# Optimization experiments

Measured on AMD Instinct MI355X. Metric: run time of the kernel, lower is better.

Reference implementation:

```python
import jax, jax.numpy as jnp
import numpy as np

N_NODES = 50000
N_EDGES = 800000
D_IN = 128
D_OUT = 128


def setup_inputs() -> dict:
    key = jax.random.key(0)
    k_x, k_r, k_c, k_v, k_w = jax.random.split(key, 5)
    x = jax.random.normal(k_x, (N_NODES, D_IN), dtype=jnp.float32)
    edge_row = jax.random.randint(k_r, (N_EDGES,), 0, N_NODES)  # destination nodes
    edge_col = jax.random.randint(k_c, (N_EDGES,), 0, N_NODES)  # source nodes
    edge_val = jax.random.uniform(k_v, (N_EDGES,), dtype=jnp.float32)
    W = jax.random.normal(k_w, (D_OUT, D_IN), dtype=jnp.float32) * (1.0 / np.sqrt(D_IN))
    bias = jnp.zeros((D_OUT,), dtype=jnp.float32)
    return {"x": x, "edge_row": edge_row, "edge_col": edge_col,
            "edge_val": edge_val, "W": W, "bias": bias}


def reference(x, edge_row, edge_col, edge_val, W, bias):
    # support = linear(x)   (nn.Linear with bias=False: x @ W.T)
    support = jnp.einsum('ni,oi->no', x, W)  # [N, D_OUT]
    # out = sparse.mm(adj, support): gather source rows, scale by edge value,
    # scatter-add into destination rows.
    msgs = edge_val[:, None] * support[edge_col]  # [E, D_OUT]
    out = jax.ops.segment_sum(msgs, edge_row, num_segments=N_NODES)
    return out + bias
```

## Files before the change

kernel.cpp:

```cpp
#include <hip/hip_runtime.h>
#include <hip/hip_bf16.h>


constexpr int D     = 128;
constexpr int NPB   = 64;
constexpr int CAP   = 2048;
constexpr int C1    = 2048;
constexpr int BT    = 1024;
constexpr int NBMAX = 1024;

__device__ inline unsigned int bf1(float f) {
    unsigned int u = __float_as_uint(f);
    return (u + 0x7fffu + ((u >> 16) & 1u)) >> 16;
}
__device__ inline unsigned int cvt2(float a, float b) {
    __hip_bfloat162 h = __float22bfloat162_rn(float2{a, b});
    return *reinterpret_cast<unsigned int*>(&h);
}
__device__ inline float bflo(unsigned int u) { return __uint_as_float(u << 16); }
__device__ inline float bfhi(unsigned int u) { return __uint_as_float(u & 0xffff0000u); }

struct BinSmem {
    int bkcnt[NBMAX];
    int bkoff[NBMAX];
    int wsum[4];
    int gbase[NBMAX];
    unsigned short slotbk[C1];
    int2 stage[C1];
};
struct GemmSmem {
    uint4 wb[2048];
};
union SmemU { BinSmem b; GemmSmem g; };

__global__ __launch_bounds__(256) void fused_gemm_bin_kernel(
        const float* __restrict__ x, const float* __restrict__ W,
        const int* __restrict__ erow, const int* __restrict__ ecol,
        const float* __restrict__ eval,
        int* __restrict__ gcursor, int2* __restrict__ coarse,
        unsigned short* __restrict__ supb,
        int n_edges, int nb, int n_nodes, int bin_blocks) {
    __shared__ SmemU sm;
    const int t = threadIdx.x;
    if ((int)blockIdx.x < bin_blocks) {
        const int base = blockIdx.x * C1;
        const int m = min(C1, n_edges - base);

        for (int i = t; i < NBMAX; i += 256) sm.b.bkcnt[i] = 0;
        __syncthreads();

        constexpr int EPT = C1 / 256;
        int  bk[EPT], rank[EPT];
        int2 pk[EPT];
#pragma unroll
        for (int j = 0; j < EPT; ++j) {
            int i = t + j * 256;
            bk[j] = -1;
            if (i < m) {
                int e = base + i;
                int dst = erow[e];
                int b = dst / NPB;
                bk[j] = b;
                rank[j] = atomicAdd(&sm.b.bkcnt[b], 1);
                pk[j] = make_int2(ecol[e] | ((dst & (NPB - 1)) << 20),
                                  __float_as_int(eval[e]));
            }
        }
        __syncthreads();

        {
            const int w = t >> 6, l = t & 63;
            const int b0 = 4 * t;
            int c0 = sm.b.bkcnt[b0], c1 = sm.b.bkcnt[b0 + 1];
            int c2 = sm.b.bkcnt[b0 + 2], c3 = sm.b.bkcnt[b0 + 3];
            int s = c0 + c1 + c2 + c3;
            int inc = s;
#pragma unroll
            for (int o = 1; o < 64; o <<= 1) {
                int u = __shfl_up(inc, o, 64);
                if (l >= o) inc += u;
            }
            if (l == 63) sm.b.wsum[w] = inc;
            __syncthreads();
            if (t < 4) {
                int v = sm.b.wsum[t];
                int winc = v;
#pragma unroll
                for (int o = 1; o < 4; o <<= 1) {
                    int u = __shfl_up(winc, o, 4);
                    if (t >= o) winc += u;
                }
                sm.b.wsum[t] = winc - v;
            }
            __syncthreads();
            int p = inc - s + sm.b.wsum[w];
            sm.b.bkoff[b0]     = p;
            sm.b.bkoff[b0 + 1] = p + c0;
            sm.b.bkoff[b0 + 2] = p + c0 + c1;
            sm.b.bkoff[b0 + 3] = p + c0 + c1 + c2;
        }
        __syncthreads();

#pragma unroll
        for (int j = 0; j < EPT; ++j) {
            if (bk[j] >= 0) {
                int s2 = sm.b.bkoff[bk[j]] + rank[j];
                sm.b.stage[s2] = pk[j];
                sm.b.slotbk[s2] = (unsigned short)bk[j];
            }
        }
        for (int i = t; i < nb; i += 256) {
            int c = sm.b.bkcnt[i];
            sm.b.gbase[i] = (c > 0) ? (i * CAP + atomicAdd(&gcursor[i], c)) : 0;
        }
        __syncthreads();

        for (int i = t; i < m; i += 256) {
            int b = sm.b.slotbk[i];
            int p = sm.b.gbase[b] + (i - sm.b.bkoff[b]);
            if (p < (b + 1) * CAP) coarse[p] = sm.b.stage[i];
        }
    } else {
        using frag  = __attribute__((ext_vector_type(8))) short;
        using f32x4 = __attribute__((ext_vector_type(4))) float;
        union FU { uint4 u; frag f; };
        const int gb = blockIdx.x - bin_blocks;
        const int wv = t >> 6;
        const int lane = t & 63;
        const int mm = lane & 15, quad = lane >> 4;
        const int row0 = gb * 64 + wv * 16;
        const int r0 = min(row0 + mm, n_nodes - 1);

        frag a[4];
#pragma unroll
        for (int kf = 0; kf < 4; ++kf) {
            const float4* xp = (const float4*)(x + (size_t)r0 * D + kf * 32 + quad * 8);
            float4 p = xp[0], q = xp[1];
            FU tu;
            tu.u.x = cvt2(p.x, p.y); tu.u.y = cvt2(p.z, p.w);
            tu.u.z = cvt2(q.x, q.y); tu.u.w = cvt2(q.z, q.w);
            a[kf] = tu.f;
        }

#pragma unroll
        for (int j = 0; j < 8; ++j) {
            int c = t + j * 256;
            int o = c >> 4, k16 = c & 15;
            const float4* wp = (const float4*)(W + (size_t)o * D + k16 * 8);
            float4 p = wp[0], q = wp[1];
            uint4 r;
            r.x = cvt2(p.x, p.y); r.y = cvt2(p.z, p.w);
            r.z = cvt2(q.x, q.y); r.w = cvt2(q.z, q.w);
            sm.g.wb[(o << 4) + (k16 ^ (o & 7))] = r;
        }
        __syncthreads();

        f32x4 acc[8];
#pragma unroll
        for (int ct = 0; ct < 8; ++ct) acc[ct] = (f32x4){0.f, 0.f, 0.f, 0.f};

#pragma unroll
        for (int ct = 0; ct < 8; ++ct) {
            const int o = ct * 16 + mm;
#pragma unroll
            for (int kf = 0; kf < 4; ++kf) {
                FU bu;
                bu.u = sm.g.wb[(o << 4) + ((kf * 4 + quad) ^ (mm & 7))];
                acc[ct] = __builtin_amdgcn_mfma_f32_16x16x32_bf16(a[kf], bu.f, acc[ct], 0, 0, 0);
            }
        }

#pragma unroll
        for (int ct = 0; ct < 8; ++ct) {
#pragma unroll
            for (int r = 0; r < 4; ++r) {
                int rr = row0 + quad * 4 + r;
                if (rr < n_nodes)
                    supb[(size_t)rr * D + ct * 16 + mm] = (unsigned short)bf1(acc[ct][r]);
            }
        }
    }
}

__global__ __launch_bounds__(BT) void sortgather_kernel(const int* __restrict__ gcursor,
                                                        const int2* __restrict__ coarse,
                                                        const unsigned short* __restrict__ supb,
                                                        const float* __restrict__ bias,
                                                        float* __restrict__ out,
                                                        int n_nodes) {
    __shared__ int ncnt[NPB];
    __shared__ int noff[NPB];
    __shared__ int ncur[NPB];
    __shared__ int2 sorted[CAP];
    const int t = threadIdx.x;
    const int b = blockIdx.x;
    const int node0 = b * NPB;
    const int m = min(gcursor[b], CAP);
    const int2* src = coarse + (size_t)b * CAP;

    if (t < NPB) ncnt[t] = 0;
    __syncthreads();

    for (int i = t; i < m; i += BT)
        atomicAdd(&ncnt[(src[i].x >> 20) & (NPB - 1)], 1);
    __syncthreads();

    if (t < NPB) {
        int v = ncnt[t];
        int inc = v;
        for (int o = 1; o < NPB; o <<= 1) {
            int u = __shfl_up(inc, o, 64);
            if (t >= o) inc += u;
        }
        noff[t] = inc - v;
        ncur[t] = inc - v;
    }
    __syncthreads();

    for (int i = t; i < m; i += BT) {
        int2 e = src[i];
        int dl = (e.x >> 20) & (NPB - 1);
        int p = atomicAdd(&ncur[dl], 1);
        sorted[p] = make_int2(e.x & 0xFFFFF, e.y);
    }
    __syncthreads();

    const int qw = t >> 4;
    const int l16 = t & 15;
    const int node = node0 + qw;
    if (node >= n_nodes) return;
    const int beg = noff[qw];
    const int end = beg + ncnt[qw];

    const float4* b4 = (const float4*)(bias + l16 * 8);
    float4 acc0 = b4[0], acc1 = b4[1];

    int e = beg;
    for (; e + 1 < end; e += 2) {
        int2 d0 = sorted[e], d1 = sorted[e + 1];
        uint4 u0 = *(const uint4*)(supb + (size_t)d0.x * D + l16 * 8);
        uint4 u1 = *(const uint4*)(supb + (size_t)d1.x * D + l16 * 8);
        float v0 = __int_as_float(d0.y), v1 = __int_as_float(d1.y);
        acc0.x += v0 * bflo(u0.x) + v1 * bflo(u1.x);
        acc0.y += v0 * bfhi(u0.x) + v1 * bfhi(u1.x);
        acc0.z += v0 * bflo(u0.y) + v1 * bflo(u1.y);
        acc0.w += v0 * bfhi(u0.y) + v1 * bfhi(u1.y);
        acc1.x += v0 * bflo(u0.z) + v1 * bflo(u1.z);
        acc1.y += v0 * bfhi(u0.z) + v1 * bfhi(u1.z);
        acc1.z += v0 * bflo(u0.w) + v1 * bflo(u1.w);
        acc1.w += v0 * bfhi(u0.w) + v1 * bfhi(u1.w);
    }
    if (e < end) {
        int2 d0 = sorted[e];
        uint4 u0 = *(const uint4*)(supb + (size_t)d0.x * D + l16 * 8);
        float v0 = __int_as_float(d0.y);
        acc0.x += v0 * bflo(u0.x); acc0.y += v0 * bfhi(u0.x);
        acc0.z += v0 * bflo(u0.y); acc0.w += v0 * bfhi(u0.y);
        acc1.x += v0 * bflo(u0.z); acc1.y += v0 * bfhi(u0.z);
        acc1.z += v0 * bflo(u0.w); acc1.w += v0 * bfhi(u0.w);
    }
    float4* o4 = (float4*)(out + (size_t)node * D + l16 * 8);
    o4[0] = acc0;
    o4[1] = acc1;
}

__global__ __launch_bounds__(256) void init_out_kernel(float4* __restrict__ out4,
                                                       const float4* __restrict__ bias4,
                                                       int total4) {
    int i = blockIdx.x * 256 + threadIdx.x;
    if (i < total4) out4[i] = bias4[i & 31];
}

__global__ __launch_bounds__(256) void scatter_fb_kernel(const int* __restrict__ erow,
                                                         const int* __restrict__ ecol,
                                                         const float* __restrict__ eval,
                                                         const unsigned short* __restrict__ supb,
                                                         float* __restrict__ out,
                                                         int n_edges) {
    int e = blockIdx.x * 8 + (threadIdx.x >> 5);
    if (e >= n_edges) return;
    int lane = threadIdx.x & 31;
    int src = ecol[e], dst = erow[e];
    float v = eval[e];
    const unsigned short* sp = supb + (size_t)src * D + lane * 4;
    float* op = out + (size_t)dst * D + lane * 4;
#pragma unroll
    for (int j = 0; j < 4; ++j)
        atomicAdd(op + j, v * __uint_as_float(((unsigned)sp[j]) << 16));
}

static inline size_t align_up(size_t v, size_t a) { return (v + a - 1) & ~(a - 1); }

extern "C" void kernel_launch(void* const* d_in, const int* in_sizes, int n_in,
                              void* d_out, int out_size, void* d_ws, size_t ws_size,
                              hipStream_t stream) {
    const float* x    = (const float*)d_in[0];
    const int*   erow = (const int*)d_in[1];
    const int*   ecol = (const int*)d_in[2];
    const float* eval = (const float*)d_in[3];
    const float* W    = (const float*)d_in[4];
    const float* bias = (const float*)d_in[5];
    float* out = (float*)d_out;

    const int n_nodes = in_sizes[0] / D;
    const int n_edges = in_sizes[1];
    const int nb = (n_nodes + NPB - 1) / NPB;

    char* base = (char*)d_ws;
    size_t off = 0;
    unsigned short* supb = (unsigned short*)(base + off); off = align_up(off + (size_t)n_nodes * D * 2, 256);
    int*  gcursor = (int*)(base + off);  off = align_up(off + (size_t)nb * 4, 256);
    int2* coarse  = (int2*)(base + off); off = align_up(off + (size_t)nb * CAP * 8, 256);

    const bool fast = (n_nodes < (1 << 20)) && (nb <= NBMAX) && (off <= ws_size);
    const int gemm_blocks = (n_nodes + 63) / 64;
    const int bin_blocks = fast ? (n_edges + C1 - 1) / C1 : 0;

    if (fast)
        hipMemsetAsync(gcursor, 0, (size_t)nb * 4, stream);

    fused_gemm_bin_kernel<<<bin_blocks + gemm_blocks, 256, 0, stream>>>(
        x, W, erow, ecol, eval, gcursor, coarse, supb,
        n_edges, nb, n_nodes, bin_blocks);

    if (fast) {
        sortgather_kernel<<<nb, BT, 0, stream>>>(
            gcursor, coarse, supb, bias, out, n_nodes);
    } else {
        int total4 = n_nodes * (D / 4);
        init_out_kernel<<<(total4 + 255) / 256, 256, 0, stream>>>(
            (float4*)out, (const float4*)bias, total4);
        scatter_fb_kernel<<<(n_edges + 7) / 8, 256, 0, stream>>>(
            erow, ecol, eval, supb, out, n_edges);
    }
}
```

Baseline: 137.6 us.

## Shrink sort-gather blocks to 256 threads and keep per-edge ranks in registers

Lowers the block size from 1024 to 256 threads, so each 16-lane group now handles four destination nodes one after another. The local counting sort now records each edge's rank from the first atomic pass in registers. The scatter into the sorted buffer then needs no second global read and no second atomic pass. The cost is fewer waves in flight for the latency-bound gather. BT is a global constant, so any other kernel that uses it also changes.

```diff
diff --git a/kernel.cpp b/kernel.cpp
--- a/kernel.cpp
+++ b/kernel.cpp
@@ -6,7 +6,7 @@
 constexpr int NPB   = 64;
 constexpr int CAP   = 2048;
 constexpr int C1    = 2048;
-constexpr int BT    = 1024;
+constexpr int BT    = 256;
 constexpr int NBMAX = 1024;
 
 __device__ inline unsigned int bf1(float f) {
@@ -190,7 +190,6 @@
                                                         int n_nodes) {
     __shared__ int ncnt[NPB];
     __shared__ int noff[NPB];
-    __shared__ int ncur[NPB];
     __shared__ int2 sorted[CAP];
     const int t = threadIdx.x;
     const int b = blockIdx.x;
@@ -201,8 +200,21 @@
     if (t < NPB) ncnt[t] = 0;
     __syncthreads();
 
-    for (int i = t; i < m; i += BT)
-        atomicAdd(&ncnt[(src[i].x >> 20) & (NPB - 1)], 1);
+    constexpr int EPT = CAP / BT;
+    int  dl[EPT], rk[EPT];
+    int2 ed[EPT];
+#pragma unroll
+    for (int j = 0; j < EPT; ++j) {
+        int i = t + j * BT;
+        dl[j] = -1;
+        if (i < m) {
+            int2 e = src[i];
+            int d = (e.x >> 20) & (NPB - 1);
+            dl[j] = d;
+            rk[j] = atomicAdd(&ncnt[d], 1);
+            ed[j] = make_int2(e.x & 0xFFFFF, e.y);
+        }
+    }
     __syncthreads();
 
     if (t < NPB) {
@@ -213,55 +225,57 @@
             if (t >= o) inc += u;
         }
         noff[t] = inc - v;
-        ncur[t] = inc - v;
     }
     __syncthreads();
 
-    for (int i = t; i < m; i += BT) {
-        int2 e = src[i];
-        int dl = (e.x >> 20) & (NPB - 1);
-        int p = atomicAdd(&ncur[dl], 1);
-        sorted[p] = make_int2(e.x & 0xFFFFF, e.y);
-    }
+#pragma unroll
+    for (int j = 0; j < EPT; ++j)
+        if (dl[j] >= 0) sorted[noff[dl[j]] + rk[j]] = ed[j];
     __syncthreads();
 
     const int qw = t >> 4;
     const int l16 = t & 15;
-    const int node = node0 + qw;
-    if (node >= n_nodes) return;
-    const int beg = noff[qw];
-    const int end = beg + ncnt[qw];
 
     const float4* b4 = (const float4*)(bias + l16 * 8);
-    float4 acc0 = b4[0], acc1 = b4[1];
-
-    int e = beg;
-    for (; e + 1 < end; e += 2) {
-        int2 d0 = sorted[e], d1 = sorted[e + 1];
-        uint4 u0 = *(const uint4*)(supb + (size_t)d0.x * D + l16 * 8);
-        uint4 u1 = *(const uint4*)(supb + (size_t)d1.x * D + l16 * 8);
-        float v0 = __int_as_float(d0.y), v1 = __int_as_float(d1.y);
-        acc0.x += v0 * bflo(u0.x) + v1 * bflo(u1.x);
-        acc0.y += v0 * bfhi(u0.x) + v1 * bfhi(u1.x);
-        acc0.z += v0 * bflo(u0.y) + v1 * bflo(u1.y);
-        acc0.w += v0 * bfhi(u0.y) + v1 * bfhi(u1.y);
-        acc1.x += v0 * bflo(u0.z) + v1 * bflo(u1.z);
-        acc1.y += v0 * bfhi(u0.z) + v1 * bfhi(u1.z);
-        acc1.z += v0 * bflo(u0.w) + v1 * bflo(u1.w);
-        acc1.w += v0 * bfhi(u0.w) + v1 * bfhi(u1.w);
-    }
-    if (e < end) {
-        int2 d0 = sorted[e];
-        uint4 u0 = *(const uint4*)(supb + (size_t)d0.x * D + l16 * 8);
-        float v0 = __int_as_float(d0.y);
-        acc0.x += v0 * bflo(u0.x); acc0.y += v0 * bfhi(u0.x);
-        acc0.z += v0 * bflo(u0.y); acc0.w += v0 * bfhi(u0.y);
-        acc1.x += v0 * bflo(u0.z); acc1.y += v0 * bfhi(u0.z);
-        acc1.z += v0 * bflo(u0.w); acc1.w += v0 * bfhi(u0.w);
-    }
-    float4* o4 = (float4*)(out + (size_t)node * D + l16 * 8);
-    o4[0] = acc0;
-    o4[1] = acc1;
+    const float4 bb0 = b4[0], bb1 = b4[1];
+
+#pragma unroll
+    for (int rep = 0; rep < 4; ++rep) {
+        const int nl = qw + rep * 16;
+        const int node = node0 + nl;
+        if (node >= n_nodes) continue;
+        const int beg = noff[nl];
+        const int end = beg + ncnt[nl];
+
+        float4 acc0 = bb0, acc1 = bb1;
+        int e = beg;
+        for (; e + 1 < end; e += 2) {
+            int2 d0 = sorted[e], d1 = sorted[e + 1];
+            uint4 u0 = *(const uint4*)(supb + (size_t)d0.x * D + l16 * 8);
+            uint4 u1 = *(const uint4*)(supb + (size_t)d1.x * D + l16 * 8);
+            float v0 = __int_as_float(d0.y), v1 = __int_as_float(d1.y);
+            acc0.x += v0 * bflo(u0.x) + v1 * bflo(u1.x);
+            acc0.y += v0 * bfhi(u0.x) + v1 * bfhi(u1.x);
+            acc0.z += v0 * bflo(u0.y) + v1 * bflo(u1.y);
+            acc0.w += v0 * bfhi(u0.y) + v1 * bfhi(u1.y);
+            acc1.x += v0 * bflo(u0.z) + v1 * bflo(u1.z);
+            acc1.y += v0 * bfhi(u0.z) + v1 * bfhi(u1.z);
+            acc1.z += v0 * bflo(u0.w) + v1 * bflo(u1.w);
+            acc1.w += v0 * bfhi(u0.w) + v1 * bfhi(u1.w);
+        }
+        if (e < end) {
+            int2 d0 = sorted[e];
+            uint4 u0 = *(const uint4*)(supb + (size_t)d0.x * D + l16 * 8);
+            float v0 = __int_as_float(d0.y);
+            acc0.x += v0 * bflo(u0.x); acc0.y += v0 * bfhi(u0.x);
+            acc0.z += v0 * bflo(u0.y); acc0.w += v0 * bfhi(u0.y);
+            acc1.x += v0 * bflo(u0.z); acc1.y += v0 * bfhi(u0.z);
+            acc1.z += v0 * bflo(u0.w); acc1.w += v0 * bfhi(u0.w);
+        }
+        float4* o4 = (float4*)(out + (size_t)node * D + l16 * 8);
+        o4[0] = acc0;
+        o4[1] = acc1;
+    }
 }
 
 __global__ __launch_bounds__(256) void init_out_kernel(float4* __restrict__ out4,
```

After: 138.9 us. No clear change (+0.9%).
